# Optimization experiments

Hardware: AMD Instinct MI355X
Metric: run time of the kernel (lower is better)

The kernel has to match this reference:

```python
import jax, jax.numpy as jnp
import numpy as np

B, N, C = 4, 2048, 128
H = 4
HD = C // H
SCALE = HD ** -0.5
NEG = -9e15


def setup_inputs() -> dict:
    key = jax.random.key(0)
    ks = jax.random.split(key, 6)
    x = jax.random.normal(ks[0], (B, N, C), dtype=jnp.float32)
    A = jax.random.randint(ks[1], (N, N), 0, 2, dtype=jnp.int32)
    std = 0.02
    Wq = jax.random.normal(ks[2], (C, C), dtype=jnp.float32) * std
    Wkv = jax.random.normal(ks[3], (2 * C, C), dtype=jnp.float32) * std
    Wp = jax.random.normal(ks[4], (C, C), dtype=jnp.float32) * std
    bp = jnp.zeros((C,), dtype=jnp.float32)
    return {"x": x, "A": A, "Wq": Wq, "Wkv": Wkv, "Wp": Wp, "bp": bp}


def reference(x, A, Wq, Wkv, Wp, bp):
    # q/k/v projections (torch Linear: x @ W.T)
    q = (x @ Wq.T).reshape(B, N, H, HD).transpose(0, 2, 1, 3)      # [B,H,N,HD]
    kv = (x @ Wkv.T).reshape(B, N, 2, H, HD).transpose(2, 0, 3, 1, 4)
    k, v = kv[0], kv[1]                                            # [B,H,N,HD]
    attn = jnp.einsum('bhnd,bhmd->bhnm', q, k) * SCALE             # [B,H,N,N]
    attn = jnp.where(A > 0, attn, NEG)                             # adjacency mask
    attn = jax.nn.softmax(attn, axis=-1)
    out = jnp.einsum('bhnm,bhmd->bhnd', attn, v)                   # [B,H,N,HD]
    out = out.transpose(0, 2, 1, 3).reshape(B, N, C)
    out = out @ Wp.T + bp
    return out + x                                                 # residual
```

## Files before the change

### kernel.cpp

```cpp
#include <hip/hip_runtime.h>
#include <math.h>

constexpr int kB = 4, kN = 2048, kC = 128, kH = 4, kHD = 32;
constexpr float kScaleLog2e = 0.17677669529663687f * 1.4426950408889634f;

typedef __attribute__((ext_vector_type(8))) short bf16x8;
typedef __attribute__((ext_vector_type(4))) float f32x4;

__device__ __forceinline__ float exp2fast(float x) { return __builtin_amdgcn_exp2f(x); }
__device__ __forceinline__ unsigned int cvtpk(float lo, float hi) {
  unsigned int r;
  asm("v_cvt_pk_bf16_f32 %0, %1, %2" : "=v"(r) : "v"(lo), "v"(hi));
  return r;
}
__device__ __forceinline__ float bflo(unsigned int u) {
  union { unsigned int u; float f; } v; v.u = u << 16; return v.f;
}
__device__ __forceinline__ float bfhi(unsigned int u) {
  union { unsigned int u; float f; } v; v.u = u & 0xFFFF0000u; return v.f;
}

__global__ __launch_bounds__(256) void prep_kernel(
    const int* __restrict__ A, const float* __restrict__ Wq,
    const float* __restrict__ Wkv, const float* __restrict__ Wp,
    unsigned long long* __restrict__ Abits, unsigned short* __restrict__ Wallb,
    unsigned short* __restrict__ Wpb) {
  const int bid = blockIdx.x;
  if (bid < 512) {
    const int lane = threadIdx.x & 63;
    const int w0 = bid * 4 + (threadIdx.x >> 6);
    for (int idx = w0; idx < kN * 32; idx += 2048) {
      const int row = idx >> 5, c0 = (idx & 31) * 64;
      unsigned long long msk = __ballot(A[(size_t)row * kN + c0 + lane] > 0);
      if (lane == 0) Abits[idx] = msk;
    }
  } else {
    const int i4 = ((bid - 512) * 256 + threadIdx.x) * 4;
    float4 v;
    unsigned short* dst;
    if (i4 < 16384) {
      v = *(const float4*)&Wq[i4];
      v.x *= kScaleLog2e; v.y *= kScaleLog2e; v.z *= kScaleLog2e; v.w *= kScaleLog2e;
      dst = Wallb + i4;
    } else if (i4 < 49152) {
      v = *(const float4*)&Wkv[i4 - 16384];
      dst = Wallb + i4;
    } else {
      v = *(const float4*)&Wp[i4 - 49152];
      dst = Wpb + (i4 - 49152);
    }
    uint2 pk = make_uint2(cvtpk(v.x, v.y), cvtpk(v.z, v.w));
    *(uint2*)dst = pk;
  }
}

__global__ __launch_bounds__(256) void qkv_kernel(
    const float* __restrict__ x, const unsigned short* __restrict__ Wallb,
    unsigned short* __restrict__ qws, unsigned short* __restrict__ kws,
    unsigned short* __restrict__ vtws) {
  __shared__ unsigned short xs[16][136];
  const int t = threadIdx.x;
  const int row0 = blockIdx.x * 16;
  const int b = row0 >> 11;
  {
    const int r = t >> 4, c = (t & 15) * 8;
    const float* src = x + (size_t)(row0 + r) * kC + c;
    float4 a = *(const float4*)src;
    float4 bb = *(const float4*)(src + 4);
    uint4 pk = make_uint4(cvtpk(a.x, a.y), cvtpk(a.z, a.w),
                          cvtpk(bb.x, bb.y), cvtpk(bb.z, bb.w));
    *(uint4*)&xs[r][c] = pk;
  }
  __syncthreads();
  const int w = t >> 6, l = t & 63, lr = l & 15, g = l >> 4;
  bf16x8 xf[4];
  #pragma unroll
  for (int s = 0; s < 4; ++s) xf[s] = *(const bf16x8*)&xs[lr][s * 32 + g * 8];
  #pragma unroll
  for (int ci = 0; ci < 6; ++ci) {
    const int c0 = (w * 6 + ci) * 16;
    const unsigned short* wr = Wallb + (size_t)(c0 + lr) * kC + g * 8;
    f32x4 acc = {0.f, 0.f, 0.f, 0.f};
    if (c0 < 256) {
      #pragma unroll
      for (int s = 0; s < 4; ++s) {
        bf16x8 wf = *(const bf16x8*)(wr + s * 32);
        acc = __builtin_amdgcn_mfma_f32_16x16x32_bf16(wf, xf[s], acc, 0, 0, 0);
      }
      const int col0 = c0 + g * 4;
      const int h = (col0 & 127) >> 5, hd0 = col0 & 31;
      unsigned short* dst = (col0 < 128) ? qws : kws;
      uint2 pk = make_uint2(cvtpk(acc[0], acc[1]), cvtpk(acc[2], acc[3]));
      *(uint2*)&dst[((size_t)(b * kH + h) * kN + row0 + lr) * kHD + hd0] = pk;
    } else {
      #pragma unroll
      for (int s = 0; s < 4; ++s) {
        bf16x8 wf = *(const bf16x8*)(wr + s * 32);
        acc = __builtin_amdgcn_mfma_f32_16x16x32_bf16(xf[s], wf, acc, 0, 0, 0);
      }
      const int d = (c0 - 256) + lr;
      uint2 pk = make_uint2(cvtpk(acc[0], acc[1]), cvtpk(acc[2], acc[3]));
      *(uint2*)&vtws[((size_t)(b * kH + (d >> 5)) * kHD + (d & 31)) * kN + row0 + g * 4] = pk;
    }
  }
}

__global__ __launch_bounds__(256) void attn_kernel(
    const unsigned short* __restrict__ qws, const unsigned short* __restrict__ kws,
    const unsigned short* __restrict__ vtws,
    const unsigned long long* __restrict__ Abits,
    unsigned short* __restrict__ Opart, float* __restrict__ lws, int tiles) {
  __shared__ unsigned short Ks[2][64][40];
  __shared__ unsigned short Vt[2][32][72];
  __shared__ unsigned short Ps[4][16][72];
  const int t = threadIdx.x, w = t >> 6, l = t & 63, lr = l & 15, g = l >> 4;
  const int bh = blockIdx.y, q0 = blockIdx.x * 64, z = blockIdx.z;
  const int q = q0 + w * 16 + lr;
  const int kt0 = z * tiles;
  const unsigned short* kbase = kws + (size_t)bh * kN * kHD;
  const unsigned short* vbase = vtws + (size_t)bh * kHD * kN;
  bf16x8 qf = *(const bf16x8*)&qws[((size_t)bh * kN + q) * kHD + g * 8];
  const unsigned long long* arow = Abits + (size_t)q * (kN / 64);
  const int ks_r = t >> 2, ks_c = (t & 3) * 8;
  const int vs_d = t >> 3, vs_c = (t & 7) * 8;
  const int gsh = g * 4;

  bf16x8 kreg = *(const bf16x8*)&kbase[(size_t)(kt0 * 64 + ks_r) * kHD + ks_c];
  bf16x8 vreg = *(const bf16x8*)&vbase[(size_t)vs_d * kN + kt0 * 64 + vs_c];
  *(bf16x8*)&Ks[0][ks_r][ks_c] = kreg;
  *(bf16x8*)&Vt[0][vs_d][vs_c] = vreg;

  float lsum = 0.f;
  f32x4 o0 = {0.f, 0.f, 0.f, 0.f}, o1 = {0.f, 0.f, 0.f, 0.f};

  for (int it = 0; it < tiles; ++it) {
    const int c = it & 1;
    const int kt = kt0 + it;
    __syncthreads();
    if (it + 1 < tiles) {
      kreg = *(const bf16x8*)&kbase[(size_t)((kt + 1) * 64 + ks_r) * kHD + ks_c];
      vreg = *(const bf16x8*)&vbase[(size_t)vs_d * kN + (kt + 1) * 64 + vs_c];
    }
    const unsigned long long mw = arow[kt];
    const unsigned int wlo = ((unsigned int)mw) >> gsh;
    const unsigned int whi = ((unsigned int)(mw >> 32)) >> gsh;

    float s[16];
    #pragma unroll
    for (int kc = 0; kc < 4; ++kc) {
      bf16x8 kf = *(const bf16x8*)&Ks[c][kc * 16 + lr][g * 8];
      f32x4 acc = {0.f, 0.f, 0.f, 0.f};
      acc = __builtin_amdgcn_mfma_f32_16x16x32_bf16(kf, qf, acc, 0, 0, 0);
      #pragma unroll
      for (int i = 0; i < 4; ++i) s[kc * 4 + i] = acc[i];
    }
    #pragma unroll
    for (int kc = 0; kc < 4; ++kc) {
      const unsigned int word = (kc < 2) ? wlo : whi;
      #pragma unroll
      for (int i = 0; i < 4; ++i) {
        float p = exp2fast(s[kc * 4 + i]);
        const int msk = ((int)(word << (31 - ((kc & 1) * 16 + i)))) >> 31;
        union { float f; int u; } pu; pu.f = p;
        pu.u &= msk;
        s[kc * 4 + i] = pu.f;
        lsum += pu.f;
      }
    }
    #pragma unroll
    for (int kc = 0; kc < 4; ++kc) {
      uint2 pk;
      pk.x = cvtpk(s[kc * 4 + 0], s[kc * 4 + 1]);
      pk.y = cvtpk(s[kc * 4 + 2], s[kc * 4 + 3]);
      *(uint2*)&Ps[w][lr][kc * 16 + g * 4] = pk;
    }
    #pragma unroll
    for (int ct = 0; ct < 2; ++ct) {
      bf16x8 pf = *(const bf16x8*)&Ps[w][lr][ct * 32 + g * 8];
      bf16x8 va = *(const bf16x8*)&Vt[c][lr][ct * 32 + g * 8];
      bf16x8 vb = *(const bf16x8*)&Vt[c][16 + lr][ct * 32 + g * 8];
      o0 = __builtin_amdgcn_mfma_f32_16x16x32_bf16(va, pf, o0, 0, 0, 0);
      o1 = __builtin_amdgcn_mfma_f32_16x16x32_bf16(vb, pf, o1, 0, 0, 0);
    }
    if (it + 1 < tiles) {
      *(bf16x8*)&Ks[c ^ 1][ks_r][ks_c] = kreg;
      *(bf16x8*)&Vt[c ^ 1][vs_d][vs_c] = vreg;
    }
  }

  lsum += __shfl_xor(lsum, 16);
  lsum += __shfl_xor(lsum, 32);
  unsigned short* orow = Opart + ((size_t)(z * 16 + bh) * kN + q) * kHD;
  uint2 wa = make_uint2(cvtpk(o0[0], o0[1]), cvtpk(o0[2], o0[3]));
  uint2 wb = make_uint2(cvtpk(o1[0], o1[1]), cvtpk(o1[2], o1[3]));
  *(uint2*)&orow[g * 4] = wa;
  *(uint2*)&orow[16 + g * 4] = wb;
  if (g == 0) lws[(size_t)(z * 16 + bh) * kN + q] = lsum;
}

__global__ __launch_bounds__(256) void proj_kernel(
    const unsigned short* __restrict__ Opart, const float* __restrict__ lws,
    const unsigned short* __restrict__ Wpb, const float* __restrict__ bp,
    const float* __restrict__ x, float* __restrict__ out, int np) {
  const int t = threadIdx.x, w = t >> 6, l = t & 63, lr = l & 15, g = l >> 4;
  const int row0 = blockIdx.x * 16;
  const int b = row0 >> 11;
  bf16x8 af[4];
  #pragma unroll
  for (int s = 0; s < 4; ++s) {
    const int bh = b * kH + s;
    float a0 = 0.f, a1 = 0.f, a2 = 0.f, a3 = 0.f, a4 = 0.f, a5 = 0.f, a6 = 0.f, a7 = 0.f;
    float lacc = 0.f;
    for (int p = 0; p < np; ++p) {
      const size_t base = (size_t)(p * 16 + bh) * kN + row0 + lr;
      const uint4 u = *(const uint4*)&Opart[base * kHD + g * 8];
      lacc += lws[base];
      a0 += bflo(u.x); a1 += bfhi(u.x);
      a2 += bflo(u.y); a3 += bfhi(u.y);
      a4 += bflo(u.z); a5 += bfhi(u.z);
      a6 += bflo(u.w); a7 += bfhi(u.w);
    }
    const float inv = 1.f / fmaxf(lacc, 1e-30f);
    union { uint4 u; bf16x8 v; } cv;
    cv.u = make_uint4(cvtpk(a0 * inv, a1 * inv), cvtpk(a2 * inv, a3 * inv),
                      cvtpk(a4 * inv, a5 * inv), cvtpk(a6 * inv, a7 * inv));
    af[s] = cv.v;
  }
  #pragma unroll
  for (int ci = 0; ci < 2; ++ci) {
    const int c0 = (w * 2 + ci) * 16;
    const unsigned short* wr = Wpb + (size_t)(c0 + lr) * kC + g * 8;
    f32x4 acc = {0.f, 0.f, 0.f, 0.f};
    #pragma unroll
    for (int s = 0; s < 4; ++s) {
      bf16x8 wf = *(const bf16x8*)(wr + s * 32);
      acc = __builtin_amdgcn_mfma_f32_16x16x32_bf16(wf, af[s], acc, 0, 0, 0);
    }
    const int col0 = c0 + g * 4;
    const size_t off = (size_t)(row0 + lr) * kC + col0;
    const float4 xb = *(const float4*)&x[off];
    const float4 bb = *(const float4*)&bp[col0];
    float4 r;
    r.x = acc[0] + bb.x + xb.x;
    r.y = acc[1] + bb.y + xb.y;
    r.z = acc[2] + bb.z + xb.z;
    r.w = acc[3] + bb.w + xb.w;
    *(float4*)&out[off] = r;
  }
}

extern "C" void kernel_launch(void* const* d_in, const int* in_sizes, int n_in,
                              void* d_out, int out_size, void* d_ws, size_t ws_size,
                              hipStream_t stream) {
  const float* x   = (const float*)d_in[0];
  const int*   A   = (const int*)d_in[1];
  const float* Wq  = (const float*)d_in[2];
  const float* Wkv = (const float*)d_in[3];
  const float* Wp  = (const float*)d_in[4];
  const float* bp  = (const float*)d_in[5];
  float* out = (float*)d_out;
  char* ws = (char*)d_ws;

  unsigned short* qws   = (unsigned short*)(ws);
  unsigned short* kws   = (unsigned short*)(ws + (2u << 20));
  unsigned short* vtws  = (unsigned short*)(ws + (4u << 20));
  unsigned long long* Abits = (unsigned long long*)(ws + (6u << 20));
  unsigned short* Wallb = (unsigned short*)(ws + (6u << 20) + (1u << 19));
  unsigned short* Wpb   = Wallb + 384 * 128;
  float*          lws   = (float*)(ws + (7u << 20));
  unsigned short* Opart = (unsigned short*)(ws + (8u << 20));

  const int np = (ws_size >= (16u << 20)) ? 4 : 1;
  const int tiles = 32 / np;

  prep_kernel<<<dim3(576), dim3(256), 0, stream>>>(A, Wq, Wkv, Wp, Abits, Wallb, Wpb);
  qkv_kernel<<<dim3(512), dim3(256), 0, stream>>>(x, Wallb, qws, kws, vtws);
  attn_kernel<<<dim3(32, 16, np), dim3(256), 0, stream>>>(
      qws, kws, vtws, Abits, Opart, lws, tiles);
  proj_kernel<<<dim3(512), dim3(256), 0, stream>>>(Opart, lws, Wpb, bp, x, out, np);
}
```

Measured before the change: 61.16 us.

## Fuse weight conversion into QKV/proj kernels, merge mask packing, restructure attention LDS

```diff
diff --git a/kernel.cpp b/kernel.cpp
--- a/kernel.cpp
+++ b/kernel.cpp
@@ -20,56 +20,33 @@
   union { unsigned int u; float f; } v; v.u = u & 0xFFFF0000u; return v.f;
 }
 
-__global__ __launch_bounds__(256) void prep_kernel(
-    const int* __restrict__ A, const float* __restrict__ Wq,
-    const float* __restrict__ Wkv, const float* __restrict__ Wp,
-    unsigned long long* __restrict__ Abits, unsigned short* __restrict__ Wallb,
-    unsigned short* __restrict__ Wpb) {
+__global__ __launch_bounds__(256) void qkv_abit_kernel(
+    const float* __restrict__ x, const float* __restrict__ Wq,
+    const float* __restrict__ Wkv, const int* __restrict__ A,
+    unsigned short* __restrict__ qws, unsigned short* __restrict__ kws,
+    unsigned short* __restrict__ vtws, unsigned long long* __restrict__ Abits) {
   const int bid = blockIdx.x;
-  if (bid < 512) {
-    const int lane = threadIdx.x & 63;
-    const int w0 = bid * 4 + (threadIdx.x >> 6);
+  const int t = threadIdx.x;
+  if (bid >= 512) {
+    const int lane = t & 63;
+    const int w0 = (bid - 512) * 4 + (t >> 6);
     for (int idx = w0; idx < kN * 32; idx += 2048) {
       const int row = idx >> 5, c0 = (idx & 31) * 64;
       unsigned long long msk = __ballot(A[(size_t)row * kN + c0 + lane] > 0);
       if (lane == 0) Abits[idx] = msk;
     }
-  } else {
-    const int i4 = ((bid - 512) * 256 + threadIdx.x) * 4;
-    float4 v;
-    unsigned short* dst;
-    if (i4 < 16384) {
-      v = *(const float4*)&Wq[i4];
-      v.x *= kScaleLog2e; v.y *= kScaleLog2e; v.z *= kScaleLog2e; v.w *= kScaleLog2e;
-      dst = Wallb + i4;
-    } else if (i4 < 49152) {
-      v = *(const float4*)&Wkv[i4 - 16384];
-      dst = Wallb + i4;
-    } else {
-      v = *(const float4*)&Wp[i4 - 49152];
-      dst = Wpb + (i4 - 49152);
-    }
-    uint2 pk = make_uint2(cvtpk(v.x, v.y), cvtpk(v.z, v.w));
-    *(uint2*)dst = pk;
-  }
-}
-
-__global__ __launch_bounds__(256) void qkv_kernel(
-    const float* __restrict__ x, const unsigned short* __restrict__ Wallb,
-    unsigned short* __restrict__ qws, unsigned short* __restrict__ kws,
-    unsigned short* __restrict__ vtws) {
+    return;
+  }
   __shared__ unsigned short xs[16][136];
-  const int t = threadIdx.x;
-  const int row0 = blockIdx.x * 16;
+  const int row0 = bid * 16;
   const int b = row0 >> 11;
   {
     const int r = t >> 4, c = (t & 15) * 8;
     const float* src = x + (size_t)(row0 + r) * kC + c;
     float4 a = *(const float4*)src;
     float4 bb = *(const float4*)(src + 4);
-    uint4 pk = make_uint4(cvtpk(a.x, a.y), cvtpk(a.z, a.w),
-                          cvtpk(bb.x, bb.y), cvtpk(bb.z, bb.w));
-    *(uint4*)&xs[r][c] = pk;
+    *(uint4*)&xs[r][c] = make_uint4(cvtpk(a.x, a.y), cvtpk(a.z, a.w),
+                                    cvtpk(bb.x, bb.y), cvtpk(bb.z, bb.w));
   }
   __syncthreads();
   const int w = t >> 6, l = t & 63, lr = l & 15, g = l >> 4;
@@ -79,13 +56,22 @@
   #pragma unroll
   for (int ci = 0; ci < 6; ++ci) {
     const int c0 = (w * 6 + ci) * 16;
-    const unsigned short* wr = Wallb + (size_t)(c0 + lr) * kC + g * 8;
+    const float* wrow = (c0 < 128) ? (Wq + (size_t)(c0 + lr) * kC)
+                                   : (Wkv + (size_t)(c0 - 128 + lr) * kC);
     f32x4 acc = {0.f, 0.f, 0.f, 0.f};
     if (c0 < 256) {
       #pragma unroll
       for (int s = 0; s < 4; ++s) {
-        bf16x8 wf = *(const bf16x8*)(wr + s * 32);
-        acc = __builtin_amdgcn_mfma_f32_16x16x32_bf16(wf, xf[s], acc, 0, 0, 0);
+        const float* wp = wrow + s * 32 + g * 8;
+        float4 wa = *(const float4*)wp, wb = *(const float4*)(wp + 4);
+        union { uint4 u; bf16x8 v; } cw;
+        cw.u = make_uint4(cvtpk(wa.x, wa.y), cvtpk(wa.z, wa.w),
+                          cvtpk(wb.x, wb.y), cvtpk(wb.z, wb.w));
+        acc = __builtin_amdgcn_mfma_f32_16x16x32_bf16(cw.v, xf[s], acc, 0, 0, 0);
+      }
+      if (c0 < 128) {
+        #pragma unroll
+        for (int i = 0; i < 4; ++i) acc[i] *= kScaleLog2e;
       }
       const int col0 = c0 + g * 4;
       const int h = (col0 & 127) >> 5, hd0 = col0 & 31;
@@ -95,8 +81,12 @@
     } else {
       #pragma unroll
       for (int s = 0; s < 4; ++s) {
-        bf16x8 wf = *(const bf16x8*)(wr + s * 32);
-        acc = __builtin_amdgcn_mfma_f32_16x16x32_bf16(xf[s], wf, acc, 0, 0, 0);
+        const float* wp = wrow + s * 32 + g * 8;
+        float4 wa = *(const float4*)wp, wb = *(const float4*)(wp + 4);
+        union { uint4 u; bf16x8 v; } cw;
+        cw.u = make_uint4(cvtpk(wa.x, wa.y), cvtpk(wa.z, wa.w),
+                          cvtpk(wb.x, wb.y), cvtpk(wb.z, wb.w));
+        acc = __builtin_amdgcn_mfma_f32_16x16x32_bf16(xf[s], cw.v, acc, 0, 0, 0);
       }
       const int d = (c0 - 256) + lr;
       uint2 pk = make_uint2(cvtpk(acc[0], acc[1]), cvtpk(acc[2], acc[3]));
@@ -110,9 +100,9 @@
     const unsigned short* __restrict__ vtws,
     const unsigned long long* __restrict__ Abits,
     unsigned short* __restrict__ Opart, float* __restrict__ lws, int tiles) {
-  __shared__ unsigned short Ks[2][64][40];
-  __shared__ unsigned short Vt[2][32][72];
-  __shared__ unsigned short Ps[4][16][72];
+  __shared__ unsigned short Ksf[2][4][64][8];
+  __shared__ unsigned short Vtf[2][2][2][64][8];
+  __shared__ unsigned short Psf[4][2][64][8];
   const int t = threadIdx.x, w = t >> 6, l = t & 63, lr = l & 15, g = l >> 4;
   const int bh = blockIdx.y, q0 = blockIdx.x * 64, z = blockIdx.z;
   const int q = q0 + w * 16 + lr;
@@ -121,86 +111,84 @@
   const unsigned short* vbase = vtws + (size_t)bh * kHD * kN;
   bf16x8 qf = *(const bf16x8*)&qws[((size_t)bh * kN + q) * kHD + g * 8];
   const unsigned long long* arow = Abits + (size_t)q * (kN / 64);
-  const int ks_r = t >> 2, ks_c = (t & 3) * 8;
-  const int vs_d = t >> 3, vs_c = (t & 7) * 8;
+
+  const int skc = t >> 6, sl = t & 63;
+  const size_t koff = ((size_t)(skc * 16 + (sl & 15))) * kHD + (sl >> 4) * 8;
+  const int sdh = t >> 7, sct = (t >> 6) & 1;
+  const size_t voff = ((size_t)(sdh * 16 + (sl & 15))) * kN + sct * 32 + (sl >> 4) * 8;
+
+  bf16x8 kreg = *(const bf16x8*)(kbase + (size_t)kt0 * 64 * kHD + koff);
+  bf16x8 vreg = *(const bf16x8*)(vbase + (size_t)kt0 * 64 + voff);
+  *(bf16x8*)&Ksf[0][skc][sl][0] = kreg;
+  *(bf16x8*)&Vtf[0][sdh][sct][sl][0] = vreg;
+  unsigned long long mw = arow[kt0], mwn = 0;
+
+  f32x4 o0 = {0.f, 0.f, 0.f, 0.f}, o1 = {0.f, 0.f, 0.f, 0.f}, o2 = {0.f, 0.f, 0.f, 0.f};
+  bf16x8 ones;
+  #pragma unroll
+  for (int i = 0; i < 8; ++i) ones[i] = (short)0x3F80;
   const int gsh = g * 4;
-
-  bf16x8 kreg = *(const bf16x8*)&kbase[(size_t)(kt0 * 64 + ks_r) * kHD + ks_c];
-  bf16x8 vreg = *(const bf16x8*)&vbase[(size_t)vs_d * kN + kt0 * 64 + vs_c];
-  *(bf16x8*)&Ks[0][ks_r][ks_c] = kreg;
-  *(bf16x8*)&Vt[0][vs_d][vs_c] = vreg;
-
-  float lsum = 0.f;
-  f32x4 o0 = {0.f, 0.f, 0.f, 0.f}, o1 = {0.f, 0.f, 0.f, 0.f};
+  unsigned short* const psw = &Psf[w][0][0][0];
+  const int pbase = (((g >> 1) << 4) | lr) * 8 + (g & 1) * 4;
 
   for (int it = 0; it < tiles; ++it) {
     const int c = it & 1;
     const int kt = kt0 + it;
     __syncthreads();
     if (it + 1 < tiles) {
-      kreg = *(const bf16x8*)&kbase[(size_t)((kt + 1) * 64 + ks_r) * kHD + ks_c];
-      vreg = *(const bf16x8*)&vbase[(size_t)vs_d * kN + (kt + 1) * 64 + vs_c];
-    }
-    const unsigned long long mw = arow[kt];
+      kreg = *(const bf16x8*)(kbase + (size_t)(kt + 1) * 64 * kHD + koff);
+      vreg = *(const bf16x8*)(vbase + (size_t)(kt + 1) * 64 + voff);
+      mwn = arow[kt + 1];
+    }
     const unsigned int wlo = ((unsigned int)mw) >> gsh;
     const unsigned int whi = ((unsigned int)(mw >> 32)) >> gsh;
 
-    float s[16];
     #pragma unroll
     for (int kc = 0; kc < 4; ++kc) {
-      bf16x8 kf = *(const bf16x8*)&Ks[c][kc * 16 + lr][g * 8];
+      bf16x8 kf = *(const bf16x8*)&Ksf[c][kc][l][0];
       f32x4 acc = {0.f, 0.f, 0.f, 0.f};
       acc = __builtin_amdgcn_mfma_f32_16x16x32_bf16(kf, qf, acc, 0, 0, 0);
-      #pragma unroll
-      for (int i = 0; i < 4; ++i) s[kc * 4 + i] = acc[i];
-    }
-    #pragma unroll
-    for (int kc = 0; kc < 4; ++kc) {
       const unsigned int word = (kc < 2) ? wlo : whi;
+      float p[4];
       #pragma unroll
       for (int i = 0; i < 4; ++i) {
-        float p = exp2fast(s[kc * 4 + i]);
-        const int msk = ((int)(word << (31 - ((kc & 1) * 16 + i)))) >> 31;
-        union { float f; int u; } pu; pu.f = p;
+        float e = exp2fast(acc[i]);
+        int msk;
+        asm("v_bfe_i32 %0, %1, %2, 1" : "=v"(msk) : "v"(word), "n"((kc & 1) * 16 + i));
+        union { float f; int u; } pu; pu.f = e;
         pu.u &= msk;
-        s[kc * 4 + i] = pu.f;
-        lsum += pu.f;
-      }
-    }
-    #pragma unroll
-    for (int kc = 0; kc < 4; ++kc) {
-      uint2 pk;
-      pk.x = cvtpk(s[kc * 4 + 0], s[kc * 4 + 1]);
-      pk.y = cvtpk(s[kc * 4 + 2], s[kc * 4 + 3]);
-      *(uint2*)&Ps[w][lr][kc * 16 + g * 4] = pk;
+        p[i] = pu.f;
+      }
+      uint2 pk = make_uint2(cvtpk(p[0], p[1]), cvtpk(p[2], p[3]));
+      *(uint2*)(psw + kc * 256 + pbase) = pk;
     }
     #pragma unroll
     for (int ct = 0; ct < 2; ++ct) {
-      bf16x8 pf = *(const bf16x8*)&Ps[w][lr][ct * 32 + g * 8];
-      bf16x8 va = *(const bf16x8*)&Vt[c][lr][ct * 32 + g * 8];
-      bf16x8 vb = *(const bf16x8*)&Vt[c][16 + lr][ct * 32 + g * 8];
+      bf16x8 pf = *(const bf16x8*)&Psf[w][ct][l][0];
+      bf16x8 va = *(const bf16x8*)&Vtf[c][0][ct][l][0];
+      bf16x8 vb = *(const bf16x8*)&Vtf[c][1][ct][l][0];
       o0 = __builtin_amdgcn_mfma_f32_16x16x32_bf16(va, pf, o0, 0, 0, 0);
       o1 = __builtin_amdgcn_mfma_f32_16x16x32_bf16(vb, pf, o1, 0, 0, 0);
+      o2 = __builtin_amdgcn_mfma_f32_16x16x32_bf16(ones, pf, o2, 0, 0, 0);
     }
     if (it + 1 < tiles) {
-      *(bf16x8*)&Ks[c ^ 1][ks_r][ks_c] = kreg;
-      *(bf16x8*)&Vt[c ^ 1][vs_d][vs_c] = vreg;
-    }
-  }
-
-  lsum += __shfl_xor(lsum, 16);
-  lsum += __shfl_xor(lsum, 32);
+      *(bf16x8*)&Ksf[c ^ 1][skc][sl][0] = kreg;
+      *(bf16x8*)&Vtf[c ^ 1][sdh][sct][sl][0] = vreg;
+      mw = mwn;
+    }
+  }
+
   unsigned short* orow = Opart + ((size_t)(z * 16 + bh) * kN + q) * kHD;
   uint2 wa = make_uint2(cvtpk(o0[0], o0[1]), cvtpk(o0[2], o0[3]));
   uint2 wb = make_uint2(cvtpk(o1[0], o1[1]), cvtpk(o1[2], o1[3]));
   *(uint2*)&orow[g * 4] = wa;
   *(uint2*)&orow[16 + g * 4] = wb;
-  if (g == 0) lws[(size_t)(z * 16 + bh) * kN + q] = lsum;
+  if (g == 0) lws[(size_t)(z * 16 + bh) * kN + q] = o2[0];
 }
 
 __global__ __launch_bounds__(256) void proj_kernel(
     const unsigned short* __restrict__ Opart, const float* __restrict__ lws,
-    const unsigned short* __restrict__ Wpb, const float* __restrict__ bp,
+    const float* __restrict__ Wp, const float* __restrict__ bp,
     const float* __restrict__ x, float* __restrict__ out, int np) {
   const int t = threadIdx.x, w = t >> 6, l = t & 63, lr = l & 15, g = l >> 4;
   const int row0 = blockIdx.x * 16;
@@ -229,12 +217,16 @@
   #pragma unroll
   for (int ci = 0; ci < 2; ++ci) {
     const int c0 = (w * 2 + ci) * 16;
-    const unsigned short* wr = Wpb + (size_t)(c0 + lr) * kC + g * 8;
+    const float* wrow = Wp + (size_t)(c0 + lr) * kC;
     f32x4 acc = {0.f, 0.f, 0.f, 0.f};
     #pragma unroll
     for (int s = 0; s < 4; ++s) {
-      bf16x8 wf = *(const bf16x8*)(wr + s * 32);
-      acc = __builtin_amdgcn_mfma_f32_16x16x32_bf16(wf, af[s], acc, 0, 0, 0);
+      const float* wp = wrow + s * 32 + g * 8;
+      float4 wa = *(const float4*)wp, wb = *(const float4*)(wp + 4);
+      union { uint4 u; bf16x8 v; } cw;
+      cw.u = make_uint4(cvtpk(wa.x, wa.y), cvtpk(wa.z, wa.w),
+                        cvtpk(wb.x, wb.y), cvtpk(wb.z, wb.w));
+      acc = __builtin_amdgcn_mfma_f32_16x16x32_bf16(cw.v, af[s], acc, 0, 0, 0);
     }
     const int col0 = c0 + g * 4;
     const size_t off = (size_t)(row0 + lr) * kC + col0;
@@ -265,17 +257,15 @@
   unsigned short* kws   = (unsigned short*)(ws + (2u << 20));
   unsigned short* vtws  = (unsigned short*)(ws + (4u << 20));
   unsigned long long* Abits = (unsigned long long*)(ws + (6u << 20));
-  unsigned short* Wallb = (unsigned short*)(ws + (6u << 20) + (1u << 19));
-  unsigned short* Wpb   = Wallb + 384 * 128;
   float*          lws   = (float*)(ws + (7u << 20));
   unsigned short* Opart = (unsigned short*)(ws + (8u << 20));
 
   const int np = (ws_size >= (16u << 20)) ? 4 : 1;
   const int tiles = 32 / np;
 
-  prep_kernel<<<dim3(576), dim3(256), 0, stream>>>(A, Wq, Wkv, Wp, Abits, Wallb, Wpb);
-  qkv_kernel<<<dim3(512), dim3(256), 0, stream>>>(x, Wallb, qws, kws, vtws);
+  qkv_abit_kernel<<<dim3(1024), dim3(256), 0, stream>>>(
+      x, Wq, Wkv, A, qws, kws, vtws, Abits);
   attn_kernel<<<dim3(32, 16, np), dim3(256), 0, stream>>>(
       qws, kws, vtws, Abits, Opart, lws, tiles);
-  proj_kernel<<<dim3(512), dim3(256), 0, stream>>>(Opart, lws, Wpb, bp, x, out, np);
-}
+  proj_kernel<<<dim3(512), dim3(256), 0, stream>>>(Opart, lws, Wp, bp, x, out, np);
+}
```

After: 66.27 us. 8.4% more time.
